# Kernel optimization log

Measured on AMD Instinct MI355X. Metric: run time of the kernel, lower is better.

## Reference

```python
import jax, jax.numpy as jnp
import numpy as np

MODEL_DIM = 4096
NUM_EXPERTS = 64
TOPK = 2
ROUTE_SCALE = 1.0


def setup_inputs() -> dict:
    key = jax.random.key(0)
    kx, kw = jax.random.split(key)
    x = jax.random.normal(kx, (16384, MODEL_DIM), dtype=jnp.float32)
    # xavier_uniform for [num_experts, model_dim]
    limit = float(np.sqrt(6.0 / (NUM_EXPERTS + MODEL_DIM)))
    weight = jax.random.uniform(kw, (NUM_EXPERTS, MODEL_DIM), dtype=jnp.float32,
                                minval=-limit, maxval=limit)
    return {"x": x, "weight": weight}


def reference(x, weight):
    # scores: [N, num_experts]
    scores = jnp.einsum('nd,ed->ne', x, weight)
    all_scores = jax.nn.softmax(scores, axis=-1)  # score_func='softmax'
    topk_vals, topk_idx = jax.lax.top_k(all_scores, TOPK)  # [N, topk]
    topk_vals = topk_vals * ROUTE_SCALE
    return (topk_vals, topk_idx, all_scores)
```

## Files before the change

kernel.cpp:

```cpp
#include <hip/hip_runtime.h>
#include <math.h>

#define N_ROWS 16384
#define DIM 4096
#define NEXP 64
#define KWAVES 8
#define KSLICE (DIM / KWAVES)
#define KC 32
#define NCHUNK (KSLICE / KC)
#define RPB 32
#define NKO (DIM / 8)

typedef short short8 __attribute__((ext_vector_type(8)));
typedef float f32x4  __attribute__((ext_vector_type(4)));

__device__ __forceinline__ unsigned cvt_pk_bf16(float a, float b) {
    unsigned r;
    asm("v_cvt_pk_bf16_f32 %0, %1, %2" : "=v"(r) : "v"(a), "v"(b));
    return r;
}

__device__ __forceinline__ void split3(const float* xv, short8& h8, short8& m8, short8& l8) {
    union { unsigned u[4]; short8 s; } H, M, L;
#pragma unroll
    for (int j = 0; j < 4; ++j) {
        float a = xv[2 * j], b = xv[2 * j + 1];
        unsigned hp = cvt_pk_bf16(a, b);
        float a1 = a - __uint_as_float(hp << 16);
        float b1 = b - __uint_as_float(hp & 0xffff0000u);
        unsigned mp = cvt_pk_bf16(a1, b1);
        float a2 = a1 - __uint_as_float(mp << 16);
        float b2 = b1 - __uint_as_float(mp & 0xffff0000u);
        H.u[j] = hp; M.u[j] = mp; L.u[j] = cvt_pk_bf16(a2, b2);
    }
    h8 = H.s; m8 = M.s; l8 = L.s;
}

__device__ __forceinline__ bool gtpair(float a, int ia, float b, int ib) {
    return (a > b) || (a == b && ia < ib);
}

__global__ __launch_bounds__(256)
void convw_kernel(const float* __restrict__ w, short8* __restrict__ w0t,
                  short8* __restrict__ w1t, short8* __restrict__ w2t)
{
    const int t  = blockIdx.x * 256 + threadIdx.x;
    const int ko = t >> 6;
    const int e  = t & 63;
    const float* src = w + (size_t)e * DIM + ko * 8;
    float xv[8];
#pragma unroll
    for (int j = 0; j < 8; ++j) xv[j] = src[j];
    short8 h, m, l;
    split3(xv, h, m, l);
    w0t[ko * 64 + e] = h;
    w1t[ko * 64 + e] = m;
    w2t[ko * 64 + e] = l;
}

__global__ __launch_bounds__(512, 4)
void gate_kernel(const float* __restrict__ x, const short8* __restrict__ w0t,
                 const short8* __restrict__ w1t, const short8* __restrict__ w2t,
                 float* __restrict__ out)
{
    __shared__ float part[KWAVES][RPB][NEXP];

    const int tid  = threadIdx.x;
    const int lane = tid & 63;
    const int wv   = tid >> 6;
    const int l15  = lane & 15;
    const int g    = lane >> 4;
    const int row0 = blockIdx.x * RPB;

    f32x4 acc[2][4];
#pragma unroll
    for (int mt = 0; mt < 2; ++mt)
#pragma unroll
        for (int nt = 0; nt < 4; ++nt) acc[mt][nt] = (f32x4){0.f, 0.f, 0.f, 0.f};

    const float* xp0 = x + (size_t)(row0 + l15) * DIM + wv * KSLICE + g * 8;
    const float* xp1 = xp0 + 16 * DIM;

    float4 c00 = *reinterpret_cast<const float4*>(xp0);
    float4 c01 = *reinterpret_cast<const float4*>(xp0 + 4);
    float4 c10 = *reinterpret_cast<const float4*>(xp1);
    float4 c11 = *reinterpret_cast<const float4*>(xp1 + 4);

    for (int t = 0; t < NCHUNK; ++t) {
        const int tn = (t < NCHUNK - 1 ? t + 1 : t) * KC;
        float4 n00 = *reinterpret_cast<const float4*>(xp0 + tn);
        float4 n01 = *reinterpret_cast<const float4*>(xp0 + tn + 4);
        float4 n10 = *reinterpret_cast<const float4*>(xp1 + tn);
        float4 n11 = *reinterpret_cast<const float4*>(xp1 + tn + 4);

        float v0[8] = {c00.x, c00.y, c00.z, c00.w, c01.x, c01.y, c01.z, c01.w};
        float v1[8] = {c10.x, c10.y, c10.z, c10.w, c11.x, c11.y, c11.z, c11.w};
        short8 a0h, a0m, a0l, a1h, a1m, a1l;
        split3(v0, a0h, a0m, a0l);
        split3(v1, a1h, a1m, a1l);

        const int base = (wv * 64 + t * 4 + g) * 64 + l15;
#pragma unroll
        for (int nt = 0; nt < 4; ++nt) {
            short8 b0 = w0t[base + nt * 16];
            short8 b1 = w1t[base + nt * 16];
            short8 b2 = w2t[base + nt * 16];
            acc[0][nt] = __builtin_amdgcn_mfma_f32_16x16x32_bf16(a0l, b0, acc[0][nt], 0, 0, 0);
            acc[0][nt] = __builtin_amdgcn_mfma_f32_16x16x32_bf16(a0m, b1, acc[0][nt], 0, 0, 0);
            acc[0][nt] = __builtin_amdgcn_mfma_f32_16x16x32_bf16(a0h, b2, acc[0][nt], 0, 0, 0);
            acc[0][nt] = __builtin_amdgcn_mfma_f32_16x16x32_bf16(a0m, b0, acc[0][nt], 0, 0, 0);
            acc[0][nt] = __builtin_amdgcn_mfma_f32_16x16x32_bf16(a0h, b1, acc[0][nt], 0, 0, 0);
            acc[0][nt] = __builtin_amdgcn_mfma_f32_16x16x32_bf16(a0h, b0, acc[0][nt], 0, 0, 0);

            acc[1][nt] = __builtin_amdgcn_mfma_f32_16x16x32_bf16(a1l, b0, acc[1][nt], 0, 0, 0);
            acc[1][nt] = __builtin_amdgcn_mfma_f32_16x16x32_bf16(a1m, b1, acc[1][nt], 0, 0, 0);
            acc[1][nt] = __builtin_amdgcn_mfma_f32_16x16x32_bf16(a1h, b2, acc[1][nt], 0, 0, 0);
            acc[1][nt] = __builtin_amdgcn_mfma_f32_16x16x32_bf16(a1m, b0, acc[1][nt], 0, 0, 0);
            acc[1][nt] = __builtin_amdgcn_mfma_f32_16x16x32_bf16(a1h, b1, acc[1][nt], 0, 0, 0);
            acc[1][nt] = __builtin_amdgcn_mfma_f32_16x16x32_bf16(a1h, b0, acc[1][nt], 0, 0, 0);
        }
        c00 = n00; c01 = n01; c10 = n10; c11 = n11;
    }

#pragma unroll
    for (int mt = 0; mt < 2; ++mt)
#pragma unroll
        for (int nt = 0; nt < 4; ++nt)
#pragma unroll
            for (int r = 0; r < 4; ++r) {
                const int rw = mt * 16 + g * 4 + r;
                const int cl = (nt * 16 + l15) ^ (((rw >> 2) & 3) << 4);
                part[wv][rw][cl] = acc[mt][nt][r];
            }
    __syncthreads();

    float* out_vals = out;
    float* out_idx  = out + (size_t)N_ROWS * 2;
    float* out_sc   = out + (size_t)N_ROWS * 4;

#pragma unroll
    for (int i = 0; i < 4; ++i) {
        const int r = wv * 4 + i;
        const int row = row0 + r;
        const int cl = lane ^ (((r >> 2) & 3) << 4);
        float s = 0.f;
#pragma unroll
        for (int kw = 0; kw < KWAVES; ++kw) s += part[kw][r][cl];
        float m = s;
#pragma unroll
        for (int off = 32; off; off >>= 1) m = fmaxf(m, __shfl_xor(m, off));
        float e = expf(s - m);
        float sum = e;
#pragma unroll
        for (int off = 32; off; off >>= 1) sum += __shfl_xor(sum, off);
        float p = e / sum;
        out_sc[(size_t)row * 64 + lane] = p;

        float v1 = p; int i1 = lane; float v2 = -1.f; int i2 = lane;
#pragma unroll
        for (int off = 32; off; off >>= 1) {
            float o1 = __shfl_xor(v1, off); int oi1 = __shfl_xor(i1, off);
            float o2 = __shfl_xor(v2, off); int oi2 = __shfl_xor(i2, off);
            if (gtpair(o1, oi1, v1, i1)) {
                if (gtpair(v1, i1, o2, oi2)) { v2 = v1; i2 = i1; }
                else                         { v2 = o2; i2 = oi2; }
                v1 = o1; i1 = oi1;
            } else if (gtpair(o1, oi1, v2, i2)) {
                v2 = o1; i2 = oi1;
            }
        }
        if (lane == 0) {
            out_vals[(size_t)row * 2 + 0] = v1;
            out_vals[(size_t)row * 2 + 1] = v2;
            out_idx[(size_t)row * 2 + 0]  = (float)i1;
            out_idx[(size_t)row * 2 + 1]  = (float)i2;
        }
    }
}

extern "C" void kernel_launch(void* const* d_in, const int* in_sizes, int n_in,
                              void* d_out, int out_size, void* d_ws, size_t ws_size,
                              hipStream_t stream)
{
    const float* x = (const float*)d_in[0];
    const float* w = (const float*)d_in[1];
    float* out = (float*)d_out;

    short8* w0t = (short8*)d_ws;
    short8* w1t = w0t + NKO * NEXP;
    short8* w2t = w1t + NKO * NEXP;

    convw_kernel<<<dim3(128), dim3(256), 0, stream>>>(w, w0t, w1t, w2t);
    gate_kernel<<<dim3(N_ROWS / RPB), dim3(512), 0, stream>>>(x, w0t, w1t, w2t, out);
}
```

Measured before the change: 87.01 us.

## Switch gate GEMM to 32x32x16 MFMA with double-buffered weight and x loads

Replaces the 16x16x32 bf16 MFMA tiling with 32x32x16 MFMAs, so each wave covers 32 rows by 64 experts using two 16-register accumulators. The weight preconversion kernel now writes the split bf16 weights in a per-step layout matched to the 32x32 operand pattern. The K loop is unrolled by two, with register double buffering of x and weight loads and sched barriers to overlap loads with MFMA work. The aim is fewer MFMA issues and better latency hiding, at the cost of more registers per thread, which may hurt occupancy under the 4-block launch bound.

```diff
diff --git a/kernel.cpp b/kernel.cpp
--- a/kernel.cpp
+++ b/kernel.cpp
@@ -6,13 +6,12 @@
 #define NEXP 64
 #define KWAVES 8
 #define KSLICE (DIM / KWAVES)
-#define KC 32
-#define NCHUNK (KSLICE / KC)
+#define NK16 (KSLICE / 16)
 #define RPB 32
-#define NKO (DIM / 8)
+#define NSTEP (DIM / 16)
 
 typedef short short8 __attribute__((ext_vector_type(8)));
-typedef float f32x4  __attribute__((ext_vector_type(4)));
+typedef float f32x16 __attribute__((ext_vector_type(16)));
 
 __device__ __forceinline__ unsigned cvt_pk_bf16(float a, float b) {
     unsigned r;
@@ -45,18 +44,21 @@
                   short8* __restrict__ w1t, short8* __restrict__ w2t)
 {
     const int t  = blockIdx.x * 256 + threadIdx.x;
-    const int ko = t >> 6;
-    const int e  = t & 63;
-    const float* src = w + (size_t)e * DIM + ko * 8;
+    const int s  = t >> 7;
+    const int nt = (t >> 6) & 1;
+    const int l  = t & 63;
+    const int e  = nt * 32 + (l & 31);
+    const int k  = s * 16 + (l >> 5) * 8;
+    const float* src = w + (size_t)e * DIM + k;
     float xv[8];
 #pragma unroll
     for (int j = 0; j < 8; ++j) xv[j] = src[j];
-    short8 h, m, l;
-    split3(xv, h, m, l);
-    w0t[ko * 64 + e] = h;
-    w1t[ko * 64 + e] = m;
-    w2t[ko * 64 + e] = l;
-}
+    short8 h, m, lo;
+    split3(xv, h, m, lo);
+    w0t[t] = h; w1t[t] = m; w2t[t] = lo;
+}
+
+#define MFMA32(A, B, C) __builtin_amdgcn_mfma_f32_32x32x16_bf16((A), (B), (C), 0, 0, 0)
 
 __global__ __launch_bounds__(512, 4)
 void gate_kernel(const float* __restrict__ x, const short8* __restrict__ w0t,
@@ -68,70 +70,76 @@
     const int tid  = threadIdx.x;
     const int lane = tid & 63;
     const int wv   = tid >> 6;
-    const int l15  = lane & 15;
-    const int g    = lane >> 4;
+    const int e31  = lane & 31;
+    const int h    = lane >> 5;
     const int row0 = blockIdx.x * RPB;
 
-    f32x4 acc[2][4];
-#pragma unroll
-    for (int mt = 0; mt < 2; ++mt)
-#pragma unroll
-        for (int nt = 0; nt < 4; ++nt) acc[mt][nt] = (f32x4){0.f, 0.f, 0.f, 0.f};
-
-    const float* xp0 = x + (size_t)(row0 + l15) * DIM + wv * KSLICE + g * 8;
-    const float* xp1 = xp0 + 16 * DIM;
-
-    float4 c00 = *reinterpret_cast<const float4*>(xp0);
-    float4 c01 = *reinterpret_cast<const float4*>(xp0 + 4);
-    float4 c10 = *reinterpret_cast<const float4*>(xp1);
-    float4 c11 = *reinterpret_cast<const float4*>(xp1 + 4);
-
-    for (int t = 0; t < NCHUNK; ++t) {
-        const int tn = (t < NCHUNK - 1 ? t + 1 : t) * KC;
-        float4 n00 = *reinterpret_cast<const float4*>(xp0 + tn);
-        float4 n01 = *reinterpret_cast<const float4*>(xp0 + tn + 4);
-        float4 n10 = *reinterpret_cast<const float4*>(xp1 + tn);
-        float4 n11 = *reinterpret_cast<const float4*>(xp1 + tn + 4);
-
-        float v0[8] = {c00.x, c00.y, c00.z, c00.w, c01.x, c01.y, c01.z, c01.w};
-        float v1[8] = {c10.x, c10.y, c10.z, c10.w, c11.x, c11.y, c11.z, c11.w};
-        short8 a0h, a0m, a0l, a1h, a1m, a1l;
-        split3(v0, a0h, a0m, a0l);
-        split3(v1, a1h, a1m, a1l);
-
-        const int base = (wv * 64 + t * 4 + g) * 64 + l15;
-#pragma unroll
-        for (int nt = 0; nt < 4; ++nt) {
-            short8 b0 = w0t[base + nt * 16];
-            short8 b1 = w1t[base + nt * 16];
-            short8 b2 = w2t[base + nt * 16];
-            acc[0][nt] = __builtin_amdgcn_mfma_f32_16x16x32_bf16(a0l, b0, acc[0][nt], 0, 0, 0);
-            acc[0][nt] = __builtin_amdgcn_mfma_f32_16x16x32_bf16(a0m, b1, acc[0][nt], 0, 0, 0);
-            acc[0][nt] = __builtin_amdgcn_mfma_f32_16x16x32_bf16(a0h, b2, acc[0][nt], 0, 0, 0);
-            acc[0][nt] = __builtin_amdgcn_mfma_f32_16x16x32_bf16(a0m, b0, acc[0][nt], 0, 0, 0);
-            acc[0][nt] = __builtin_amdgcn_mfma_f32_16x16x32_bf16(a0h, b1, acc[0][nt], 0, 0, 0);
-            acc[0][nt] = __builtin_amdgcn_mfma_f32_16x16x32_bf16(a0h, b0, acc[0][nt], 0, 0, 0);
-
-            acc[1][nt] = __builtin_amdgcn_mfma_f32_16x16x32_bf16(a1l, b0, acc[1][nt], 0, 0, 0);
-            acc[1][nt] = __builtin_amdgcn_mfma_f32_16x16x32_bf16(a1m, b1, acc[1][nt], 0, 0, 0);
-            acc[1][nt] = __builtin_amdgcn_mfma_f32_16x16x32_bf16(a1h, b2, acc[1][nt], 0, 0, 0);
-            acc[1][nt] = __builtin_amdgcn_mfma_f32_16x16x32_bf16(a1m, b0, acc[1][nt], 0, 0, 0);
-            acc[1][nt] = __builtin_amdgcn_mfma_f32_16x16x32_bf16(a1h, b1, acc[1][nt], 0, 0, 0);
-            acc[1][nt] = __builtin_amdgcn_mfma_f32_16x16x32_bf16(a1h, b0, acc[1][nt], 0, 0, 0);
-        }
-        c00 = n00; c01 = n01; c10 = n10; c11 = n11;
-    }
-
-#pragma unroll
-    for (int mt = 0; mt < 2; ++mt)
-#pragma unroll
-        for (int nt = 0; nt < 4; ++nt)
-#pragma unroll
-            for (int r = 0; r < 4; ++r) {
-                const int rw = mt * 16 + g * 4 + r;
-                const int cl = (nt * 16 + l15) ^ (((rw >> 2) & 3) << 4);
-                part[wv][rw][cl] = acc[mt][nt][r];
-            }
+    f32x16 acc0 = {0.f}, acc1 = {0.f};
+#pragma unroll
+    for (int j = 0; j < 16; ++j) { acc0[j] = 0.f; acc1[j] = 0.f; }
+
+    const float* xp = x + (size_t)(row0 + e31) * DIM + wv * KSLICE + h * 8;
+
+    short8 wA0, wA1, wA2, wA3, wA4, wA5;
+    short8 wB0, wB1, wB2, wB3, wB4, wB5;
+    float4 xA0, xA1, xB0, xB1;
+
+#define LOADW(p0, p1, p2, p3, p4, p5, S)                                       \
+    do {                                                                       \
+        const int _i = ((wv * NK16 + (S)) * 2) * 64 + lane;                    \
+        p0 = w0t[_i];      p1 = w1t[_i];      p2 = w2t[_i];                    \
+        p3 = w0t[_i + 64]; p4 = w1t[_i + 64]; p5 = w2t[_i + 64];               \
+    } while (0)
+
+#define LOADX(d0, d1, S)                                                       \
+    do {                                                                       \
+        d0 = *reinterpret_cast<const float4*>(xp + (S) * 16);                  \
+        d1 = *reinterpret_cast<const float4*>(xp + (S) * 16 + 4);              \
+    } while (0)
+
+#define DOSTEP(X0, X1, q0, q1, q2, q3, q4, q5)                                 \
+    do {                                                                       \
+        float xv[8] = {X0.x, X0.y, X0.z, X0.w, X1.x, X1.y, X1.z, X1.w};        \
+        short8 ah, am, al;                                                     \
+        split3(xv, ah, am, al);                                                \
+        acc0 = MFMA32(al, q0, acc0);                                           \
+        acc0 = MFMA32(am, q1, acc0);                                           \
+        acc0 = MFMA32(ah, q2, acc0);                                           \
+        acc0 = MFMA32(am, q0, acc0);                                           \
+        acc0 = MFMA32(ah, q1, acc0);                                           \
+        acc0 = MFMA32(ah, q0, acc0);                                           \
+        acc1 = MFMA32(al, q3, acc1);                                           \
+        acc1 = MFMA32(am, q4, acc1);                                           \
+        acc1 = MFMA32(ah, q5, acc1);                                           \
+        acc1 = MFMA32(am, q3, acc1);                                           \
+        acc1 = MFMA32(ah, q4, acc1);                                           \
+        acc1 = MFMA32(ah, q3, acc1);                                           \
+    } while (0)
+
+    LOADW(wA0, wA1, wA2, wA3, wA4, wA5, 0); LOADX(xA0, xA1, 0);
+    LOADW(wB0, wB1, wB2, wB3, wB4, wB5, 1); LOADX(xB0, xB1, 1);
+
+    for (int t = 0; t < NK16; t += 2) {
+        DOSTEP(xA0, xA1, wA0, wA1, wA2, wA3, wA4, wA5);
+        {
+            const int t2 = (t + 2) & (NK16 - 1);
+            LOADW(wA0, wA1, wA2, wA3, wA4, wA5, t2); LOADX(xA0, xA1, t2);
+        }
+        __builtin_amdgcn_sched_barrier(0);
+        DOSTEP(xB0, xB1, wB0, wB1, wB2, wB3, wB4, wB5);
+        {
+            const int t3 = (t + 3) & (NK16 - 1);
+            LOADW(wB0, wB1, wB2, wB3, wB4, wB5, t3); LOADX(xB0, xB1, t3);
+        }
+        __builtin_amdgcn_sched_barrier(0);
+    }
+
+#pragma unroll
+    for (int reg = 0; reg < 16; ++reg) {
+        const int rw = (reg & 3) + 8 * (reg >> 2) + 4 * h;
+        part[wv][rw][e31]      = acc0[reg];
+        part[wv][rw][32 + e31] = acc1[reg];
+    }
     __syncthreads();
 
     float* out_vals = out;
@@ -142,10 +150,9 @@
     for (int i = 0; i < 4; ++i) {
         const int r = wv * 4 + i;
         const int row = row0 + r;
-        const int cl = lane ^ (((r >> 2) & 3) << 4);
         float s = 0.f;
 #pragma unroll
-        for (int kw = 0; kw < KWAVES; ++kw) s += part[kw][r][cl];
+        for (int kw = 0; kw < KWAVES; ++kw) s += part[kw][r][lane];
         float m = s;
 #pragma unroll
         for (int off = 32; off; off >>= 1) m = fmaxf(m, __shfl_xor(m, off));
@@ -187,8 +194,8 @@
     float* out = (float*)d_out;
 
     short8* w0t = (short8*)d_ws;
-    short8* w1t = w0t + NKO * NEXP;
-    short8* w2t = w1t + NKO * NEXP;
+    short8* w1t = w0t + (size_t)NSTEP * 2 * 64;
+    short8* w2t = w1t + (size_t)NSTEP * 2 * 64;
 
     convw_kernel<<<dim3(128), dim3(256), 0, stream>>>(w, w0t, w1t, w2t);
     gate_kernel<<<dim3(N_ROWS / RPB), dim3(512), 0, stream>>>(x, w0t, w1t, w2t, out);
```

Result: slower. 99.55 us (+14.4%).
